# Performance work log

Hardware: AMD Instinct MI355X
Metric: run time of the kernel (lower is better)

Reference implementation:

```python
import jax, jax.numpy as jnp
import numpy as np

# Dims: T=out_seq_len, B=batch, D=hidden_dim, H=hidden_dim_de, E=embedding_size, C=feat_channels
T, B, D, H, E, C, FH, FW = 32, 16, 512, 512, 512, 512, 8, 32


def _lstm_dir(x_seq, W_ih, W_hh, b_ih, b_hh, reverse):
    # x_seq: (T, B, D); PyTorch gate order i, f, g, o
    gx = jnp.einsum('tbd,gd->tbg', x_seq, W_ih) + b_ih  # (T, B, 4H)
    Hh = W_hh.shape[1]
    def step(carry, g_t):
        h, c = carry
        g = g_t + h @ W_hh.T + b_hh
        i, f, gg, o = jnp.split(g, 4, axis=-1)
        c = jax.nn.sigmoid(f) * c + jax.nn.sigmoid(i) * jnp.tanh(gg)
        h = jax.nn.sigmoid(o) * jnp.tanh(c)
        return (h, c), h
    init = (jnp.zeros((x_seq.shape[1], Hh), x_seq.dtype),
            jnp.zeros((x_seq.shape[1], Hh), x_seq.dtype))
    _, hs = jax.lax.scan(step, init, gx, reverse=reverse)
    return hs  # (T, B, H)


def setup_inputs() -> dict:
    key = jax.random.key(0)
    ks = jax.random.split(key, 16)
    s = 0.02
    inp = {
        'hidden_en': jax.random.normal(ks[0], (T, B, D), jnp.float32),
        'conv_f': jax.random.normal(ks[1], (B, C, FH, FW), jnp.float32),
        # bidirectional LSTM params (PyTorch layout: W_ih (4H, D), W_hh (4H, H))
        'W_ih_f': jax.random.normal(ks[2], (4 * H, D), jnp.float32) * s,
        'W_hh_f': jax.random.normal(ks[3], (4 * H, H), jnp.float32) * s,
        'b_ih_f': jnp.zeros((4 * H,), jnp.float32),
        'b_hh_f': jnp.zeros((4 * H,), jnp.float32),
        'W_ih_b': jax.random.normal(ks[4], (4 * H, D), jnp.float32) * s,
        'W_hh_b': jax.random.normal(ks[5], (4 * H, H), jnp.float32) * s,
        'b_ih_b': jnp.zeros((4 * H,), jnp.float32),
        'b_hh_b': jnp.zeros((4 * H,), jnp.float32),
        # linear_decode: (H, 2H)
        'W_dec': jax.random.normal(ks[6], (H, 2 * H), jnp.float32) * s,
        'b_dec': jnp.zeros((H,), jnp.float32),
        # conv_em: 3x3, C -> E (OIHW)
        'W_em': jax.random.normal(ks[7], (E, C, 3, 3), jnp.float32) * s,
        'b_em': jnp.zeros((E,), jnp.float32),
        # attention h_em: 1x1 conv == linear H -> E
        'W_hem': jax.random.normal(ks[8], (E, H), jnp.float32) * s,
        'b_hem': jnp.zeros((E,), jnp.float32),
        # conv_att: 1x1 conv E -> 1
        'w_att': jax.random.normal(ks[9], (E,), jnp.float32) * s,
        'b_att': jnp.zeros((), jnp.float32),
    }
    return inp


def reference(hidden_en, conv_f, W_ih_f, W_hh_f, b_ih_f, b_hh_f,
              W_ih_b, W_hh_b, b_ih_b, b_hh_b, W_dec, b_dec,
              W_em, b_em, W_hem, b_hem, w_att, b_att):
    # decoder_ctc: bidirectional LSTM + linear
    h_fwd = _lstm_dir(hidden_en, W_ih_f, W_hh_f, b_ih_f, b_hh_f, reverse=False)
    h_bwd = _lstm_dir(hidden_en, W_ih_b, W_hh_b, b_ih_b, b_hh_b, reverse=True)
    hidden_de = jnp.concatenate([h_fwd, h_bwd], axis=-1) @ W_dec.T + b_dec  # (T, B, H)

    # conv_em: 3x3 same-padding conv, NCHW
    x_em = jax.lax.conv_general_dilated(
        conv_f, W_em, window_strides=(1, 1), padding='SAME',
        dimension_numbers=('NCHW', 'OIHW', 'NCHW')) + b_em[None, :, None, None]  # (B,E,FH,FW)
    att_x_em = jnp.transpose(x_em.reshape(x_em.shape[0], E, -1), (0, 2, 1))  # (B, HW, E)

    # batched attention over all timesteps (dropout is identity at eval)
    h_em = jnp.einsum('tbh,eh->tbe', hidden_de, W_hem) + b_hem  # (T, B, E)
    feat = jnp.tanh(x_em[None] + h_em[:, :, :, None, None])     # (T, B, E, FH, FW)
    scores = jnp.einsum('tbehw,e->tbhw', feat, w_att) + b_att   # (T, B, FH, FW)
    alpha = jax.nn.softmax(scores.reshape(scores.shape[0], scores.shape[1], -1), axis=-1)  # (T,B,HW)
    att = jnp.einsum('tbn,bne->tbe', alpha, att_x_em)           # (T, B, E)

    ctc_out = jnp.concatenate([hidden_de, att], axis=-1)        # (T, B, H+E)
    return jnp.transpose(ctc_out, (1, 0, 2))                    # (B, T, H+E)
```

## Files before the change

kernel.cpp:

```cpp
#include <hip/hip_runtime.h>
#include <hip/hip_bf16.h>
#include <math.h>

#define T_LEN 32
#define BATCH 16
#define DDIM  512
#define HDIM  512
#define EDIM  512
#define CDIM  512
#define FHH   8
#define FWW   32
#define HW    256
#define G4    2048
#define PADH  10
#define PADW  34
#define WLP   520

typedef __attribute__((ext_vector_type(8))) short bf16x8;
typedef __attribute__((ext_vector_type(4))) float f32x4;

__device__ __forceinline__ ushort bfr(float x) {
    union { float f; uint32_t u; } c; c.f = x;
    uint32_t r = (c.u + 0x7FFFu + ((c.u >> 16) & 1u)) >> 16;
    return (ushort)r;
}

__device__ __forceinline__ float frcp(float x) { return __builtin_amdgcn_rcpf(x); }
__device__ __forceinline__ float ftanh(float x) {
    return 1.f - 2.f * frcp(1.f + __expf(2.f * x));
}
__device__ __forceinline__ float fsig(float x) {
    return frcp(1.f + __expf(-x));
}

__device__ __forceinline__ void ld_lds16(const void* g, void* l) {
    __builtin_amdgcn_global_load_lds((const __attribute__((address_space(1))) void*)g,
                                     (__attribute__((address_space(3))) void*)l, 16, 0, 0);
}

__device__ __forceinline__ void st_u16_sc1(ushort* p, ushort v) {
    asm volatile("global_store_short %0, %1, off sc1" :: "v"(p), "v"((uint)v) : "memory");
}
__device__ __forceinline__ void st_i32_sc1(int* p, int v) {
    asm volatile("global_store_dword %0, %1, off sc1" :: "v"(p), "v"(v) : "memory");
}
__device__ __forceinline__ int ld_i32_sc1(const int* p) {
    int v;
    asm volatile("global_load_dword %0, %1, off sc1\n\ts_waitcnt vmcnt(0)"
                 : "=v"(v) : "v"(p) : "memory");
    return v;
}


__global__ void zero_padT(ushort* __restrict__ dst) {
    int i = blockIdx.x * 256 + threadIdx.x;
    const int n = BATCH * PADH * PADW * CDIM / 4;
    if (i < n) ((ushort4*)dst)[i] = make_ushort4(0, 0, 0, 0);
}

__global__ __launch_bounds__(256) void fill_padT(const float* __restrict__ src,
                                                 ushort* __restrict__ dst) {
    __shared__ float tile[32][33];
    int s0 = blockIdx.x * 32, c0 = blockIdx.y * 32, b = blockIdx.z;
    int tid = threadIdx.x;
    int lo = tid & 31, hi = tid >> 5;
#pragma unroll
    for (int it = 0; it < 4; ++it) {
        int cl = hi + it * 8;
        tile[cl][lo] = src[((size_t)(b * CDIM + c0 + cl)) * HW + s0 + lo];
    }
    __syncthreads();
#pragma unroll
    for (int it = 0; it < 4; ++it) {
        int sl = hi + it * 8;
        int s = s0 + sl;
        int y = s >> 5, x = s & 31;
        dst[(((size_t)b * PADH + y + 1) * PADW + (x + 1)) * CDIM + c0 + lo] = bfr(tile[lo][sl]);
    }
}

__global__ void repack_wem(const float* __restrict__ src, ushort* __restrict__ dst) {
    int idx = blockIdx.x * 256 + threadIdx.x;
    const int total = 9 * EDIM * CDIM;
    if (idx >= total) return;
    int c = idx % CDIM;
    int t = idx / CDIM;
    int e = t % EDIM;
    int tap = t / EDIM;
    int dy = tap / 3, dx = tap % 3;
    dst[idx] = bfr(src[((e * CDIM + c) * 3 + dy) * 3 + dx]);
}

struct PrepArgs { const float* s[7]; ushort* d[7]; };
__global__ void fuse_prep(PrepArgs a, int* __restrict__ flags) {
    int i = blockIdx.x * 256 + threadIdx.x;
    if (i < 64) st_i32_sc1(flags + i, 0);
    const int e0 = 65536, e1 = 327680, e2 = 589824, e3 = 851968,
              e4 = 1114112, e5 = 1245184, e6 = 1310720;
    int seg, base;
    if      (i < e0) { seg = 0; base = 0;  }
    else if (i < e1) { seg = 1; base = e0; }
    else if (i < e2) { seg = 2; base = e1; }
    else if (i < e3) { seg = 3; base = e2; }
    else if (i < e4) { seg = 4; base = e3; }
    else if (i < e5) { seg = 5; base = e4; }
    else if (i < e6) { seg = 6; base = e5; }
    else return;
    int li = i - base;
    float4 v = ((const float4*)a.s[seg])[li];
    ushort4 o;
    o.x = bfr(v.x); o.y = bfr(v.y); o.z = bfr(v.z); o.w = bfr(v.w);
    ((ushort4*)a.d[seg])[li] = o;
}

__global__ __launch_bounds__(256) void gemm64(
    const ushort* __restrict__ A, const ushort* __restrict__ B,
    const float* __restrict__ bias0, const float* __restrict__ bias1,
    float* __restrict__ C, ushort* __restrict__ Cbf, float* __restrict__ Cscat,
    int M, int N, int K)
{
    __shared__ ushort As[2048], Bs[2048];
    const int n0 = blockIdx.x * 64, m0 = blockIdx.y * 64;
    const int tid = threadIdx.x, w = tid >> 6, lane = tid & 63;
    const int r0 = tid >> 2, c0 = (tid & 3) * 8;
    const ushort* Ap = A + (size_t)(m0 + r0) * K + c0;
    const ushort* Bp = B + (size_t)(n0 + r0) * K + c0;
    ushort* AsW = &As[w * 512];
    ushort* BsW = &Bs[w * 512];
    const int wm = (w >> 1) * 32, wn = (w & 1) * 32;
    const int kb = (lane >> 4) * 8, fr = lane & 15;
    f32x4 acc[2][2];
#pragma unroll
    for (int i = 0; i < 2; ++i)
#pragma unroll
        for (int j = 0; j < 2; ++j) acc[i][j] = {0.f, 0.f, 0.f, 0.f};
    for (int kk = 0; kk < K; kk += 32) {
        __syncthreads();
        ld_lds16(Ap + kk, AsW);
        ld_lds16(Bp + kk, BsW);
        __syncthreads();
        bf16x8 af[2], bg[2];
#pragma unroll
        for (int i = 0; i < 2; ++i)
            af[i] = *(const bf16x8*)&As[(wm + i * 16 + fr) * 32 + kb];
#pragma unroll
        for (int j = 0; j < 2; ++j)
            bg[j] = *(const bf16x8*)&Bs[(wn + j * 16 + fr) * 32 + kb];
#pragma unroll
        for (int i = 0; i < 2; ++i)
#pragma unroll
            for (int j = 0; j < 2; ++j)
                acc[i][j] = __builtin_amdgcn_mfma_f32_16x16x32_bf16(af[i], bg[j], acc[i][j], 0, 0, 0);
    }
    const int col = lane & 15, rq = (lane >> 4) * 4;
#pragma unroll
    for (int i = 0; i < 2; ++i) {
#pragma unroll
        for (int r = 0; r < 4; ++r) {
            int m = m0 + wm + i * 16 + rq + r;
#pragma unroll
            for (int j = 0; j < 2; ++j) {
                int n = n0 + wn + j * 16 + col;
                float v = acc[i][j][r];
                if (bias0) v += bias0[n];
                if (bias1) v += bias1[n];
                if (C)   C[(size_t)m * N + n] = v;
                if (Cbf) Cbf[(size_t)m * N + n] = bfr(v);
                if (Cscat) {
                    int t = m >> 4, b = m & 15;
                    Cscat[((size_t)(b * T_LEN + t)) * 1024 + n] = v;
                }
            }
        }
    }
}

__global__ __launch_bounds__(256) void lstm_conv(
    const ushort* __restrict__ Whh_f, const ushort* __restrict__ Whh_b,
    const float* __restrict__ gx_f, const float* __restrict__ gx_b,
    ushort* __restrict__ hs_bf,
    int* __restrict__ flags,
    const ushort* __restrict__ padT, const ushort* __restrict__ Wt,
    const float* __restrict__ bias_em, float* __restrict__ xem)
{
    __shared__ ushort smem[64 * WLP];
    const int bid = blockIdx.x, tid = threadIdx.x;
    const int w = tid >> 6, lane = tid & 63;

    if (bid < 64) {
        const int dir = bid >> 5;
        const int j0 = (bid & 31) * 16;
        const ushort* W = dir ? Whh_b : Whh_f;
        const float* gx = dir ? gx_b : gx_f;
#pragma unroll
        for (int i = 0; i < 16; ++i) {
            int row = w * 16 + i;
            int g = row >> 4, jl = row & 15;
            bf16x8 v = *(const bf16x8*)(W + ((size_t)(g * 512 + j0 + jl)) * 512 + lane * 8);
            *(bf16x8*)&smem[row * WLP + lane * 8] = v;
        }
        __syncthreads();
        if (tid >= 64) return;
        __builtin_amdgcn_s_setprio(1);

        const int fr = lane & 15, kq = lane >> 4;
        const int j = j0 + fr;
        const int fbase = dir * 32;
        const int* fq = &flags[fbase + (lane & 31)];
        f32x4 cr = {0.f, 0.f, 0.f, 0.f};
        for (int step = 0; step < T_LEN; ++step) {
            const int tcur = dir ? (T_LEN - 1 - step) : step;
            float gxv[4][4];
#pragma unroll
            for (int r = 0; r < 4; ++r) {
                const float* gxr = gx + ((size_t)tcur * BATCH + (kq * 4 + r)) * G4 + j;
#pragma unroll
                for (int g = 0; g < 4; ++g) gxv[r][g] = gxr[g * 512];
            }
            f32x4 acc[4];
#pragma unroll
            for (int g = 0; g < 4; ++g) acc[g] = {0.f, 0.f, 0.f, 0.f};
            if (step > 0) {
                const int tprev = dir ? tcur + 1 : tcur - 1;
                const ushort* hp = hs_bf + ((size_t)tprev * BATCH + fr) * 1024 + dir * 512 + kq * 8;
                bf16x8 hreg[16];
#pragma unroll
                for (int u = 0; u < 16; ++u)
                    asm volatile("global_load_dwordx4 %0, %1, off sc1"
                                 : "=v"(hreg[u]) : "v"(hp + u * 32));
                asm volatile("s_waitcnt vmcnt(0)" ::: "memory");
                __builtin_amdgcn_sched_barrier(0);
#pragma unroll
                for (int u = 0; u < 16; ++u) {
#pragma unroll
                    for (int g = 0; g < 4; ++g) {
                        bf16x8 bb = *(const bf16x8*)&smem[(g * 16 + fr) * WLP + kq * 8 + u * 32];
                        acc[g] = __builtin_amdgcn_mfma_f32_16x16x32_bf16(hreg[u], bb, acc[g], 0, 0, 0);
                    }
                }
            }
#pragma unroll
            for (int r = 0; r < 4; ++r) {
                int b = kq * 4 + r;
                float gi = gxv[r][0] + acc[0][r];
                float gf = gxv[r][1] + acc[1][r];
                float gg = gxv[r][2] + acc[2][r];
                float go = gxv[r][3] + acc[3][r];
                float si = fsig(gi), sf = fsig(gf), so = fsig(go);
                float c = sf * cr[r] + si * ftanh(gg);
                cr[r] = c;
                float h = so * ftanh(c);
                st_u16_sc1(hs_bf + ((size_t)tcur * BATCH + b) * 1024 + dir * 512 + j, bfr(h));
            }
            if (step < T_LEN - 1) {
                asm volatile("s_waitcnt vmcnt(0)" ::: "memory");
                if (lane == 0) st_i32_sc1(&flags[bid], step + 1);
                const int need = step + 1;
                for (;;) {
                    int v = ld_i32_sc1(fq);
                    if (__all(v >= need)) break;
                    __builtin_amdgcn_s_sleep(1);
                }
            }
        }
        return;
    }

    ushort* As = smem;
    ushort* Bs = smem + 2048;
    const int cbid = bid - 64;
    const int n0 = (cbid & 7) * 64, m0 = (cbid >> 3) * 64;
    const int r0 = tid >> 2, c0 = (tid & 3) * 8;
    const int b = m0 >> 8, s0 = m0 & 255, y0 = s0 >> 5;
    const int y = y0 + (r0 >> 5), x = r0 & 31;
    const ushort* Abase = padT + (((size_t)b * PADH + y) * PADW + x) * CDIM + c0;
    const ushort* Bbase = Wt + (size_t)(n0 + r0) * CDIM + c0;
    ushort* AsW = &As[w * 512];
    ushort* BsW = &Bs[w * 512];
    const int wm = (w >> 1) * 32, wn = (w & 1) * 32;
    const int kb = (lane >> 4) * 8, fr = lane & 15;
    f32x4 acc[2][2];
#pragma unroll
    for (int i = 0; i < 2; ++i)
#pragma unroll
        for (int j = 0; j < 2; ++j) acc[i][j] = {0.f, 0.f, 0.f, 0.f};
    for (int tap = 0; tap < 9; ++tap) {
        const int dy = tap / 3, dx = tap % 3;
        const ushort* ap = Abase + ((size_t)dy * PADW + dx) * CDIM;
        const ushort* bp = Bbase + (size_t)tap * EDIM * CDIM;
        for (int kk = 0; kk < CDIM; kk += 32) {
            __syncthreads();
            ld_lds16(ap + kk, AsW);
            ld_lds16(bp + kk, BsW);
            __syncthreads();
            bf16x8 af[2], bg[2];
#pragma unroll
            for (int i = 0; i < 2; ++i)
                af[i] = *(const bf16x8*)&As[(wm + i * 16 + fr) * 32 + kb];
#pragma unroll
            for (int j = 0; j < 2; ++j)
                bg[j] = *(const bf16x8*)&Bs[(wn + j * 16 + fr) * 32 + kb];
#pragma unroll
            for (int i = 0; i < 2; ++i)
#pragma unroll
                for (int j = 0; j < 2; ++j)
                    acc[i][j] = __builtin_amdgcn_mfma_f32_16x16x32_bf16(af[i], bg[j], acc[i][j], 0, 0, 0);
        }
    }
    const int col = lane & 15, rq = (lane >> 4) * 4;
#pragma unroll
    for (int i = 0; i < 2; ++i) {
#pragma unroll
        for (int r = 0; r < 4; ++r) {
            int m = m0 + wm + i * 16 + rq + r;
            int s = m & 255;
#pragma unroll
            for (int j = 0; j < 2; ++j) {
                int e = n0 + wn + j * 16 + col;
                xem[((size_t)b * EDIM + e) * HW + s] = acc[i][j][r] + bias_em[e];
            }
        }
    }
}

__global__ __launch_bounds__(256) void attention(
    const float* __restrict__ xem,
    const float* __restrict__ hem,
    const float* __restrict__ watt,
    float* __restrict__ out) {
    int i = blockIdx.x;
    int k = i >> 3;
    int b = ((i & 7) << 1) | (k & 1);
    int t = k >> 1;
    int tb = t * 16 + b;
    int tid = threadIdx.x;
    __shared__ float hl[512], wl[512], al[256], red[8];
    for (int q = tid; q < 512; q += 256) { hl[q] = hem[(size_t)tb * 512 + q]; wl[q] = watt[q]; }
    __syncthreads();
    const float* xb = xem + (size_t)b * EDIM * HW;
    float sc = 0.f;
#pragma unroll 4
    for (int e = 0; e < 512; ++e)
        sc += ftanh(xb[(size_t)e * HW + tid] + hl[e]) * wl[e];
    float m = sc;
#pragma unroll
    for (int o = 32; o; o >>= 1) m = fmaxf(m, __shfl_xor(m, o));
    if ((tid & 63) == 0) red[tid >> 6] = m;
    __syncthreads();
    m = fmaxf(fmaxf(red[0], red[1]), fmaxf(red[2], red[3]));
    float ex = __expf(sc - m);
    float s = ex;
#pragma unroll
    for (int o = 32; o; o >>= 1) s += __shfl_xor(s, o);
    if ((tid & 63) == 0) red[4 + (tid >> 6)] = s;
    __syncthreads();
    s = red[4] + red[5] + red[6] + red[7];
    al[tid] = ex * frcp(s);
    __syncthreads();
    float* ob = out + ((size_t)(b * T_LEN + t)) * 1024 + 512;
    for (int eo = 0; eo < 512; eo += 256) {
        int e = eo + tid;
        const float* xr = xb + (size_t)e * HW;
        float acc = 0.f;
#pragma unroll 4
        for (int n = 0; n < 256; n += 4) {
            float4 v = *(const float4*)&xr[n];
            acc += al[n] * v.x + al[n + 1] * v.y + al[n + 2] * v.z + al[n + 3] * v.w;
        }
        ob[e] = acc;
    }
}

extern "C" void kernel_launch(void* const* d_in, const int* in_sizes, int n_in,
                              void* d_out, int out_size, void* d_ws, size_t ws_size,
                              hipStream_t stream) {
    const float* hidden_en = (const float*)d_in[0];
    const float* conv_f    = (const float*)d_in[1];
    const float* W_ih_f    = (const float*)d_in[2];
    const float* W_hh_f    = (const float*)d_in[3];
    const float* b_ih_f    = (const float*)d_in[4];
    const float* b_hh_f    = (const float*)d_in[5];
    const float* W_ih_b    = (const float*)d_in[6];
    const float* W_hh_b    = (const float*)d_in[7];
    const float* b_ih_b    = (const float*)d_in[8];
    const float* b_hh_b    = (const float*)d_in[9];
    const float* W_dec     = (const float*)d_in[10];
    const float* b_dec     = (const float*)d_in[11];
    const float* W_em      = (const float*)d_in[12];
    const float* b_em      = (const float*)d_in[13];
    const float* W_hem     = (const float*)d_in[14];
    const float* b_hem     = (const float*)d_in[15];
    const float* w_att     = (const float*)d_in[16];
    float* out = (float*)d_out;

    char* p = (char*)d_ws;
    auto alloc = [&](size_t bytes) { void* r = p; p += (bytes + 255) & ~(size_t)255; return r; };
    float*    gx_f    = (float*)alloc((size_t)T_LEN * BATCH * G4 * 4);
    float*    gx_b    = (float*)alloc((size_t)T_LEN * BATCH * G4 * 4);
    float*    h_em    = (float*)alloc((size_t)T_LEN * BATCH * 512 * 4);
    float*    x_em    = (float*)alloc((size_t)BATCH * EDIM * HW * 4);
    ushort*   padT    = (ushort*)alloc((size_t)BATCH * PADH * PADW * CDIM * 2);
    ushort*   Wt      = (ushort*)alloc((size_t)9 * EDIM * CDIM * 2);
    ushort*   hen_bf  = (ushort*)alloc((size_t)T_LEN * BATCH * DDIM * 2);
    ushort*   Wihf_bf = (ushort*)alloc((size_t)G4 * DDIM * 2);
    ushort*   Wihb_bf = (ushort*)alloc((size_t)G4 * DDIM * 2);
    ushort*   Whhf_bf = (ushort*)alloc((size_t)G4 * HDIM * 2);
    ushort*   Whhb_bf = (ushort*)alloc((size_t)G4 * HDIM * 2);
    ushort*   Wdec_bf = (ushort*)alloc((size_t)HDIM * 1024 * 2);
    ushort*   Whem_bf = (ushort*)alloc((size_t)EDIM * HDIM * 2);
    ushort*   hs_bf   = (ushort*)alloc((size_t)T_LEN * BATCH * 1024 * 2);
    ushort*   hde_bf  = (ushort*)alloc((size_t)T_LEN * BATCH * 512 * 2);
    int*      flags   = (int*)alloc(256);

    PrepArgs pa;
    pa.s[0] = hidden_en; pa.d[0] = hen_bf;
    pa.s[1] = W_ih_f;    pa.d[1] = Wihf_bf;
    pa.s[2] = W_ih_b;    pa.d[2] = Wihb_bf;
    pa.s[3] = W_hh_f;    pa.d[3] = Whhf_bf;
    pa.s[4] = W_hh_b;    pa.d[4] = Whhb_bf;
    pa.s[5] = W_dec;     pa.d[5] = Wdec_bf;
    pa.s[6] = W_hem;     pa.d[6] = Whem_bf;
    fuse_prep<<<5120, 256, 0, stream>>>(pa, flags);
    zero_padT<<<(BATCH * PADH * PADW * CDIM / 4 + 255) / 256, 256, 0, stream>>>(padT);
    fill_padT<<<dim3(8, 16, 16), 256, 0, stream>>>(conv_f, padT);
    repack_wem<<<(9 * EDIM * CDIM + 255) / 256, 256, 0, stream>>>(W_em, Wt);

    gemm64<<<dim3(32, 8), 256, 0, stream>>>(hen_bf, Wihf_bf, b_ih_f, b_hh_f,
                                            gx_f, nullptr, nullptr, 512, G4, 512);
    gemm64<<<dim3(32, 8), 256, 0, stream>>>(hen_bf, Wihb_bf, b_ih_b, b_hh_b,
                                            gx_b, nullptr, nullptr, 512, G4, 512);

    lstm_conv<<<576, 256, 0, stream>>>(Whhf_bf, Whhb_bf, gx_f, gx_b, hs_bf, flags,
                                       padT, Wt, b_em, x_em);

    gemm64<<<dim3(8, 8), 256, 0, stream>>>(hs_bf, Wdec_bf, b_dec, nullptr,
                                           nullptr, hde_bf, out, 512, 512, 1024);

    gemm64<<<dim3(8, 8), 256, 0, stream>>>(hde_bf, Whem_bf, b_hem, nullptr,
                                           h_em, nullptr, nullptr, 512, 512, 512);

    attention<<<512, 256, 0, stream>>>(x_em, h_em, w_att, out);
}
```

Measured before the change: 273.4 us.

## Fuse input-projection GEMMs into LSTM kernel with per-timestep-tile readiness counters

The four prep kernels merge into one launch, and the padding zeroing now writes only the border cells. The two input-projection GEMMs move into the persistent LSTM/conv kernel as extra blocks. They publish finished 64-row tiles through atomic counters that the recurrent blocks poll before consuming gx, and the forward and backward directions compute tiles in the order they are consumed. This removes several launches and lets the recurrence start before all of gx is ready. The cost is spin-wait polling and a dependence on co-residency of producer and consumer blocks.

```diff
diff --git a/kernel.cpp b/kernel.cpp
--- a/kernel.cpp
+++ b/kernel.cpp
@@ -44,6 +44,9 @@
 __device__ __forceinline__ void st_i32_sc1(int* p, int v) {
     asm volatile("global_store_dword %0, %1, off sc1" :: "v"(p), "v"(v) : "memory");
 }
+__device__ __forceinline__ void st_f32_sc1(float* p, float v) {
+    asm volatile("global_store_dword %0, %1, off sc1" :: "v"(p), "v"(v) : "memory");
+}
 __device__ __forceinline__ int ld_i32_sc1(const int* p) {
     int v;
     asm volatile("global_load_dword %0, %1, off sc1\n\ts_waitcnt vmcnt(0)"
@@ -51,93 +54,94 @@
     return v;
 }
 
-
-__global__ void zero_padT(ushort* __restrict__ dst) {
-    int i = blockIdx.x * 256 + threadIdx.x;
-    const int n = BATCH * PADH * PADW * CDIM / 4;
-    if (i < n) ((ushort4*)dst)[i] = make_ushort4(0, 0, 0, 0);
-}
-
-__global__ __launch_bounds__(256) void fill_padT(const float* __restrict__ src,
-                                                 ushort* __restrict__ dst) {
+struct PrepArgs { const float* s[7]; ushort* d[7]; };
+__global__ __launch_bounds__(256) void prep_all(
+    PrepArgs a, int* __restrict__ syncbuf,
+    const float* __restrict__ conv_f, ushort* __restrict__ padT,
+    const float* __restrict__ W_em, ushort* __restrict__ Wt)
+{
     __shared__ float tile[32][33];
-    int s0 = blockIdx.x * 32, c0 = blockIdx.y * 32, b = blockIdx.z;
-    int tid = threadIdx.x;
-    int lo = tid & 31, hi = tid >> 5;
-#pragma unroll
-    for (int it = 0; it < 4; ++it) {
-        int cl = hi + it * 8;
-        tile[cl][lo] = src[((size_t)(b * CDIM + c0 + cl)) * HW + s0 + lo];
-    }
-    __syncthreads();
-#pragma unroll
-    for (int it = 0; it < 4; ++it) {
-        int sl = hi + it * 8;
-        int s = s0 + sl;
-        int y = s >> 5, x = s & 31;
-        dst[(((size_t)b * PADH + y + 1) * PADW + (x + 1)) * CDIM + c0 + lo] = bfr(tile[lo][sl]);
-    }
-}
-
-__global__ void repack_wem(const float* __restrict__ src, ushort* __restrict__ dst) {
-    int idx = blockIdx.x * 256 + threadIdx.x;
-    const int total = 9 * EDIM * CDIM;
-    if (idx >= total) return;
-    int c = idx % CDIM;
-    int t = idx / CDIM;
-    int e = t % EDIM;
-    int tap = t / EDIM;
-    int dy = tap / 3, dx = tap % 3;
-    dst[idx] = bfr(src[((e * CDIM + c) * 3 + dy) * 3 + dx]);
-}
-
-struct PrepArgs { const float* s[7]; ushort* d[7]; };
-__global__ void fuse_prep(PrepArgs a, int* __restrict__ flags) {
-    int i = blockIdx.x * 256 + threadIdx.x;
-    if (i < 64) st_i32_sc1(flags + i, 0);
-    const int e0 = 65536, e1 = 327680, e2 = 589824, e3 = 851968,
-              e4 = 1114112, e5 = 1245184, e6 = 1310720;
-    int seg, base;
-    if      (i < e0) { seg = 0; base = 0;  }
-    else if (i < e1) { seg = 1; base = e0; }
-    else if (i < e2) { seg = 2; base = e1; }
-    else if (i < e3) { seg = 3; base = e2; }
-    else if (i < e4) { seg = 4; base = e3; }
-    else if (i < e5) { seg = 5; base = e4; }
-    else if (i < e6) { seg = 6; base = e5; }
-    else return;
-    int li = i - base;
-    float4 v = ((const float4*)a.s[seg])[li];
-    ushort4 o;
-    o.x = bfr(v.x); o.y = bfr(v.y); o.z = bfr(v.z); o.w = bfr(v.w);
-    ((ushort4*)a.d[seg])[li] = o;
-}
-
-__global__ __launch_bounds__(256) void gemm64(
-    const ushort* __restrict__ A, const ushort* __restrict__ B,
-    const float* __restrict__ bias0, const float* __restrict__ bias1,
-    float* __restrict__ C, ushort* __restrict__ Cbf, float* __restrict__ Cscat,
-    int M, int N, int K)
+    const int bid = blockIdx.x, tid = threadIdx.x;
+    if (bid < 5120) {
+        int i = bid * 256 + tid;
+        if (i < 80) st_i32_sc1(syncbuf + i, 0);
+        const int e0 = 65536, e1 = 327680, e2 = 589824, e3 = 851968,
+                  e4 = 1114112, e5 = 1245184;
+        int seg, base;
+        if      (i < e0) { seg = 0; base = 0;  }
+        else if (i < e1) { seg = 1; base = e0; }
+        else if (i < e2) { seg = 2; base = e1; }
+        else if (i < e3) { seg = 3; base = e2; }
+        else if (i < e4) { seg = 4; base = e3; }
+        else if (i < e5) { seg = 5; base = e4; }
+        else             { seg = 6; base = e5; }
+        int li = i - base;
+        float4 v = ((const float4*)a.s[seg])[li];
+        ushort4 o;
+        o.x = bfr(v.x); o.y = bfr(v.y); o.z = bfr(v.z); o.w = bfr(v.w);
+        ((ushort4*)a.d[seg])[li] = o;
+        return;
+    }
+    if (bid < 7168) {
+        int id = bid - 5120;
+        int s0 = (id & 7) * 32, c0 = ((id >> 3) & 15) * 32, b = id >> 7;
+        int lo = tid & 31, hi = tid >> 5;
+#pragma unroll
+        for (int it = 0; it < 4; ++it) {
+            int cl = hi + it * 8;
+            tile[cl][lo] = conv_f[((size_t)(b * CDIM + c0 + cl)) * HW + s0 + lo];
+        }
+        __syncthreads();
+#pragma unroll
+        for (int it = 0; it < 4; ++it) {
+            int sl = hi + it * 8;
+            int s = s0 + sl;
+            int y = s >> 5, x = s & 31;
+            padT[(((size_t)b * PADH + y + 1) * PADW + (x + 1)) * CDIM + c0 + lo] =
+                bfr(tile[lo][sl]);
+        }
+        return;
+    }
+    if (bid < 7840) {
+        int gid = (bid - 7168) * 256 + tid;
+        int c4 = gid & 127;
+        int cellb = gid >> 7;
+        int cell = cellb % 84;
+        int b = cellb / 84;
+        int y, x;
+        if (cell < 34) { y = 0; x = cell; }
+        else if (cell < 68) { y = 9; x = cell - 34; }
+        else { int k2 = cell - 68; y = 1 + (k2 >> 1); x = (k2 & 1) ? 33 : 0; }
+        ((ushort4*)padT)[(((size_t)b * PADH + y) * PADW + x) * (CDIM / 4) + c4] =
+            make_ushort4(0, 0, 0, 0);
+        return;
+    }
+    {
+        int gid = (bid - 7840) * 256 + tid;
+        int c = gid % CDIM;
+        int t = gid / CDIM;
+        int e = t % EDIM;
+        int tap = t / EDIM;
+        int dy = tap / 3, dx = tap % 3;
+        Wt[gid] = bfr(W_em[((e * CDIM + c) * 3 + dy) * 3 + dx]);
+    }
+}
+
+__device__ __forceinline__ void tile64_compute(
+    const ushort* Ap0, const ushort* Bp0, int K,
+    ushort* smem, int tid, f32x4 (&acc)[2][2])
 {
-    __shared__ ushort As[2048], Bs[2048];
-    const int n0 = blockIdx.x * 64, m0 = blockIdx.y * 64;
-    const int tid = threadIdx.x, w = tid >> 6, lane = tid & 63;
-    const int r0 = tid >> 2, c0 = (tid & 3) * 8;
-    const ushort* Ap = A + (size_t)(m0 + r0) * K + c0;
-    const ushort* Bp = B + (size_t)(n0 + r0) * K + c0;
+    ushort* As = smem;
+    ushort* Bs = smem + 2048;
+    const int w = tid >> 6, lane = tid & 63;
     ushort* AsW = &As[w * 512];
     ushort* BsW = &Bs[w * 512];
     const int wm = (w >> 1) * 32, wn = (w & 1) * 32;
     const int kb = (lane >> 4) * 8, fr = lane & 15;
-    f32x4 acc[2][2];
-#pragma unroll
-    for (int i = 0; i < 2; ++i)
-#pragma unroll
-        for (int j = 0; j < 2; ++j) acc[i][j] = {0.f, 0.f, 0.f, 0.f};
     for (int kk = 0; kk < K; kk += 32) {
         __syncthreads();
-        ld_lds16(Ap + kk, AsW);
-        ld_lds16(Bp + kk, BsW);
+        ld_lds16(Ap0 + kk, AsW);
+        ld_lds16(Bp0 + kk, BsW);
         __syncthreads();
         bf16x8 af[2], bg[2];
 #pragma unroll
@@ -152,6 +156,26 @@
             for (int j = 0; j < 2; ++j)
                 acc[i][j] = __builtin_amdgcn_mfma_f32_16x16x32_bf16(af[i], bg[j], acc[i][j], 0, 0, 0);
     }
+}
+
+__global__ __launch_bounds__(256) void gemm64(
+    const ushort* __restrict__ A, const ushort* __restrict__ B,
+    const float* __restrict__ bias0,
+    float* __restrict__ C, ushort* __restrict__ Cbf, float* __restrict__ Cscat,
+    int M, int N, int K)
+{
+    __shared__ ushort smem[4096];
+    const int n0 = blockIdx.x * 64, m0 = blockIdx.y * 64;
+    const int tid = threadIdx.x, w = tid >> 6, lane = tid & 63;
+    const int r0 = tid >> 2, c0 = (tid & 3) * 8;
+    f32x4 acc[2][2];
+#pragma unroll
+    for (int i = 0; i < 2; ++i)
+#pragma unroll
+        for (int j = 0; j < 2; ++j) acc[i][j] = {0.f, 0.f, 0.f, 0.f};
+    tile64_compute(A + (size_t)(m0 + r0) * K + c0, B + (size_t)(n0 + r0) * K + c0,
+                   K, smem, tid, acc);
+    const int wm = (w >> 1) * 32, wn = (w & 1) * 32;
     const int col = lane & 15, rq = (lane >> 4) * 4;
 #pragma unroll
     for (int i = 0; i < 2; ++i) {
@@ -163,7 +187,6 @@
                 int n = n0 + wn + j * 16 + col;
                 float v = acc[i][j][r];
                 if (bias0) v += bias0[n];
-                if (bias1) v += bias1[n];
                 if (C)   C[(size_t)m * N + n] = v;
                 if (Cbf) Cbf[(size_t)m * N + n] = bfr(v);
                 if (Cscat) {
@@ -175,17 +198,23 @@
     }
 }
 
-__global__ __launch_bounds__(256) void lstm_conv(
+__global__ __launch_bounds__(256) void fused_main(
     const ushort* __restrict__ Whh_f, const ushort* __restrict__ Whh_b,
-    const float* __restrict__ gx_f, const float* __restrict__ gx_b,
+    float* __restrict__ gx_f, float* __restrict__ gx_b,
+    const ushort* __restrict__ hen_bf,
+    const ushort* __restrict__ Wih_f, const ushort* __restrict__ Wih_b,
+    const float* __restrict__ b_ih_f, const float* __restrict__ b_hh_f,
+    const float* __restrict__ b_ih_b, const float* __restrict__ b_hh_b,
     ushort* __restrict__ hs_bf,
-    int* __restrict__ flags,
+    int* __restrict__ syncbuf,
     const ushort* __restrict__ padT, const ushort* __restrict__ Wt,
     const float* __restrict__ bias_em, float* __restrict__ xem)
 {
     __shared__ ushort smem[64 * WLP];
     const int bid = blockIdx.x, tid = threadIdx.x;
     const int w = tid >> 6, lane = tid & 63;
+    int* flags = syncbuf;
+    int* gcnt  = syncbuf + 64;
 
     if (bid < 64) {
         const int dir = bid >> 5;
@@ -205,17 +234,29 @@
 
         const int fr = lane & 15, kq = lane >> 4;
         const int j = j0 + fr;
-        const int fbase = dir * 32;
-        const int* fq = &flags[fbase + (lane & 31)];
+        const int* fq = &flags[dir * 32 + (lane & 31)];
         f32x4 cr = {0.f, 0.f, 0.f, 0.f};
+        int mt_done = -1;
         for (int step = 0; step < T_LEN; ++step) {
             const int tcur = dir ? (T_LEN - 1 - step) : step;
+            const int mt = tcur >> 2;
+            if (mt != mt_done) {
+                const int* gp = &gcnt[dir * 8 + mt];
+                for (;;) {
+                    int v = ld_i32_sc1(gp);
+                    if (v >= 32) break;
+                    __builtin_amdgcn_s_sleep(4);
+                }
+                mt_done = mt;
+            }
             float gxv[4][4];
 #pragma unroll
             for (int r = 0; r < 4; ++r) {
                 const float* gxr = gx + ((size_t)tcur * BATCH + (kq * 4 + r)) * G4 + j;
 #pragma unroll
-                for (int g = 0; g < 4; ++g) gxv[r][g] = gxr[g * 512];
+                for (int g = 0; g < 4; ++g)
+                    asm volatile("global_load_dword %0, %1, off sc1"
+                                 : "=v"(gxv[r][g]) : "v"(gxr + g * 512));
             }
             f32x4 acc[4];
 #pragma unroll
@@ -238,6 +279,9 @@
                         acc[g] = __builtin_amdgcn_mfma_f32_16x16x32_bf16(hreg[u], bb, acc[g], 0, 0, 0);
                     }
                 }
+            } else {
+                asm volatile("s_waitcnt vmcnt(0)" ::: "memory");
+                __builtin_amdgcn_sched_barrier(0);
             }
 #pragma unroll
             for (int r = 0; r < 4; ++r) {
@@ -266,60 +310,77 @@
         return;
     }
 
-    ushort* As = smem;
-    ushort* Bs = smem + 2048;
-    const int cbid = bid - 64;
-    const int n0 = (cbid & 7) * 64, m0 = (cbid >> 3) * 64;
-    const int r0 = tid >> 2, c0 = (tid & 3) * 8;
-    const int b = m0 >> 8, s0 = m0 & 255, y0 = s0 >> 5;
-    const int y = y0 + (r0 >> 5), x = r0 & 31;
-    const ushort* Abase = padT + (((size_t)b * PADH + y) * PADW + x) * CDIM + c0;
-    const ushort* Bbase = Wt + (size_t)(n0 + r0) * CDIM + c0;
-    ushort* AsW = &As[w * 512];
-    ushort* BsW = &Bs[w * 512];
-    const int wm = (w >> 1) * 32, wn = (w & 1) * 32;
-    const int kb = (lane >> 4) * 8, fr = lane & 15;
-    f32x4 acc[2][2];
-#pragma unroll
-    for (int i = 0; i < 2; ++i)
-#pragma unroll
-        for (int j = 0; j < 2; ++j) acc[i][j] = {0.f, 0.f, 0.f, 0.f};
-    for (int tap = 0; tap < 9; ++tap) {
-        const int dy = tap / 3, dx = tap % 3;
-        const ushort* ap = Abase + ((size_t)dy * PADW + dx) * CDIM;
-        const ushort* bp = Bbase + (size_t)tap * EDIM * CDIM;
-        for (int kk = 0; kk < CDIM; kk += 32) {
-            __syncthreads();
-            ld_lds16(ap + kk, AsW);
-            ld_lds16(bp + kk, BsW);
-            __syncthreads();
-            bf16x8 af[2], bg[2];
-#pragma unroll
-            for (int i = 0; i < 2; ++i)
-                af[i] = *(const bf16x8*)&As[(wm + i * 16 + fr) * 32 + kb];
-#pragma unroll
-            for (int j = 0; j < 2; ++j)
-                bg[j] = *(const bf16x8*)&Bs[(wn + j * 16 + fr) * 32 + kb];
-#pragma unroll
-            for (int i = 0; i < 2; ++i)
-#pragma unroll
-                for (int j = 0; j < 2; ++j)
-                    acc[i][j] = __builtin_amdgcn_mfma_f32_16x16x32_bf16(af[i], bg[j], acc[i][j], 0, 0, 0);
-        }
-    }
-    const int col = lane & 15, rq = (lane >> 4) * 4;
-#pragma unroll
-    for (int i = 0; i < 2; ++i) {
-#pragma unroll
-        for (int r = 0; r < 4; ++r) {
-            int m = m0 + wm + i * 16 + rq + r;
-            int s = m & 255;
-#pragma unroll
-            for (int j = 0; j < 2; ++j) {
-                int e = n0 + wn + j * 16 + col;
-                xem[((size_t)b * EDIM + e) * HW + s] = acc[i][j][r] + bias_em[e];
-            }
-        }
+    if (bid < 576) {
+        const int gi = bid - 64;
+        const int dir = gi & 1;
+        const int q = gi >> 1;
+        const int nt = q & 31;
+        const int mt0 = q >> 5;
+        const int mtile = dir ? (7 - mt0) : mt0;
+        const ushort* Bw = dir ? Wih_b : Wih_f;
+        const float* bi0 = dir ? b_ih_b : b_ih_f;
+        const float* bi1 = dir ? b_hh_b : b_hh_f;
+        float* Cg = dir ? gx_b : gx_f;
+        const int m0 = mtile * 64, n0 = nt * 64;
+        const int r0 = tid >> 2, c0 = (tid & 3) * 8;
+        f32x4 acc[2][2];
+#pragma unroll
+        for (int i = 0; i < 2; ++i)
+#pragma unroll
+            for (int j = 0; j < 2; ++j) acc[i][j] = {0.f, 0.f, 0.f, 0.f};
+        tile64_compute(hen_bf + (size_t)(m0 + r0) * 512 + c0,
+                       Bw + (size_t)(n0 + r0) * 512 + c0, 512, smem, tid, acc);
+        const int wm = (w >> 1) * 32, wn = (w & 1) * 32;
+        const int col = lane & 15, rq = (lane >> 4) * 4;
+#pragma unroll
+        for (int i = 0; i < 2; ++i)
+#pragma unroll
+            for (int r = 0; r < 4; ++r) {
+                int m = m0 + wm + i * 16 + rq + r;
+#pragma unroll
+                for (int j2 = 0; j2 < 2; ++j2) {
+                    int n = n0 + wn + j2 * 16 + col;
+                    st_f32_sc1(&Cg[(size_t)m * G4 + n], acc[i][j2][r] + bi0[n] + bi1[n]);
+                }
+            }
+        asm volatile("s_waitcnt vmcnt(0)" ::: "memory");
+        __syncthreads();
+        if (tid == 0) atomicAdd(&gcnt[dir * 8 + mtile], 1);
+        return;
+    }
+
+    {
+        const int cbid = bid - 576;
+        const int n0 = (cbid & 7) * 64, m0 = (cbid >> 3) * 64;
+        const int r0 = tid >> 2, c0 = (tid & 3) * 8;
+        const int b = m0 >> 8, s0 = m0 & 255, y0 = s0 >> 5;
+        const int y = y0 + (r0 >> 5), x = r0 & 31;
+        const ushort* Abase = padT + (((size_t)b * PADH + y) * PADW + x) * CDIM + c0;
+        const ushort* Bbase = Wt + (size_t)(n0 + r0) * CDIM + c0;
+        f32x4 acc[2][2];
+#pragma unroll
+        for (int i = 0; i < 2; ++i)
+#pragma unroll
+            for (int j = 0; j < 2; ++j) acc[i][j] = {0.f, 0.f, 0.f, 0.f};
+        for (int tap = 0; tap < 9; ++tap) {
+            const int dy = tap / 3, dx = tap % 3;
+            tile64_compute(Abase + ((size_t)dy * PADW + dx) * CDIM,
+                           Bbase + (size_t)tap * EDIM * CDIM, 512, smem, tid, acc);
+        }
+        const int wm = (w >> 1) * 32, wn = (w & 1) * 32;
+        const int col = lane & 15, rq = (lane >> 4) * 4;
+#pragma unroll
+        for (int i = 0; i < 2; ++i)
+#pragma unroll
+            for (int r = 0; r < 4; ++r) {
+                int m = m0 + wm + i * 16 + rq + r;
+                int s = m & 255;
+#pragma unroll
+                for (int j2 = 0; j2 < 2; ++j2) {
+                    int e = n0 + wn + j2 * 16 + col;
+                    xem[((size_t)b * EDIM + e) * HW + s] = acc[i][j2][r] + bias_em[e];
+                }
+            }
     }
 }
 
@@ -410,7 +471,7 @@
     ushort*   Whem_bf = (ushort*)alloc((size_t)EDIM * HDIM * 2);
     ushort*   hs_bf   = (ushort*)alloc((size_t)T_LEN * BATCH * 1024 * 2);
     ushort*   hde_bf  = (ushort*)alloc((size_t)T_LEN * BATCH * 512 * 2);
-    int*      flags   = (int*)alloc(256);
+    int*      syncbuf = (int*)alloc(512);
 
     PrepArgs pa;
     pa.s[0] = hidden_en; pa.d[0] = hen_bf;
@@ -420,23 +481,17 @@
     pa.s[4] = W_hh_b;    pa.d[4] = Whhb_bf;
     pa.s[5] = W_dec;     pa.d[5] = Wdec_bf;
     pa.s[6] = W_hem;     pa.d[6] = Whem_bf;
-    fuse_prep<<<5120, 256, 0, stream>>>(pa, flags);
-    zero_padT<<<(BATCH * PADH * PADW * CDIM / 4 + 255) / 256, 256, 0, stream>>>(padT);
-    fill_padT<<<dim3(8, 16, 16), 256, 0, stream>>>(conv_f, padT);
-    repack_wem<<<(9 * EDIM * CDIM + 255) / 256, 256, 0, stream>>>(W_em, Wt);
-
-    gemm64<<<dim3(32, 8), 256, 0, stream>>>(hen_bf, Wihf_bf, b_ih_f, b_hh_f,
-                                            gx_f, nullptr, nullptr, 512, G4, 512);
-    gemm64<<<dim3(32, 8), 256, 0, stream>>>(hen_bf, Wihb_bf, b_ih_b, b_hh_b,
-                                            gx_b, nullptr, nullptr, 512, G4, 512);
-
-    lstm_conv<<<576, 256, 0, stream>>>(Whhf_bf, Whhb_bf, gx_f, gx_b, hs_bf, flags,
-                                       padT, Wt, b_em, x_em);
-
-    gemm64<<<dim3(8, 8), 256, 0, stream>>>(hs_bf, Wdec_bf, b_dec, nullptr,
+    prep_all<<<17056, 256, 0, stream>>>(pa, syncbuf, conv_f, padT, W_em, Wt);
+
+    fused_main<<<1088, 256, 0, stream>>>(Whhf_bf, Whhb_bf, gx_f, gx_b, hen_bf,
+                                         Wihf_bf, Wihb_bf, b_ih_f, b_hh_f,
+                                         b_ih_b, b_hh_b, hs_bf, syncbuf,
+                                         padT, Wt, b_em, x_em);
+
+    gemm64<<<dim3(8, 8), 256, 0, stream>>>(hs_bf, Wdec_bf, b_dec,
                                            nullptr, hde_bf, out, 512, 512, 1024);
 
-    gemm64<<<dim3(8, 8), 256, 0, stream>>>(hde_bf, Whem_bf, b_hem, nullptr,
+    gemm64<<<dim3(8, 8), 256, 0, stream>>>(hde_bf, Whem_bf, b_hem,
                                            h_em, nullptr, nullptr, 512, 512, 512);
 
     attention<<<512, 256, 0, stream>>>(x_em, h_em, w_att, out);
```

Result: faster. 253.1 us (-7.4%).
